# Kernel tuning notes

Measured on AMD Instinct MI355X. Metric: run time of the kernel, lower is better.

## Reference

```python
import jax, jax.numpy as jnp
import numpy as np

D = 256      # input channels
DK = 64      # key/query/value channels
BS, W, H = 8, 64, 64


def setup_inputs() -> dict:
    key = jax.random.key(0)
    k1, k2, k3, k4 = jax.random.split(key, 4)
    v = jax.random.normal(k1, (BS, D, W, H), dtype=jnp.float32)
    # conv1x1 weights collapse to plain matrices over the channel dim
    Wqkv = jax.random.normal(k2, (3 * DK, D), dtype=jnp.float32) * 0.02
    Wout = jax.random.normal(k3, (D, DK), dtype=jnp.float32) * 0.02
    gamma = jax.random.normal(k4, (1,), dtype=jnp.float32)  # original inits to 0; nonzero for a non-degenerate baseline
    return {"v": v, "Wqkv": Wqkv, "Wout": Wout, "gamma": gamma}


def reference(v, Wqkv, Wout, gamma):
    bs, c, w, h = v.shape
    n = w * h
    d_k = Wout.shape[1]
    x = v.reshape(bs, c, n)                      # (b, c, n)
    qkv = jnp.einsum('oc,bcn->bon', Wqkv, x)      # 1x1 conv == channel matmul
    q = qkv[:, :d_k]                              # (b, dk, n)
    k = qkv[:, d_k:2 * d_k]
    val = qkv[:, 2 * d_k:]
    s = jnp.einsum('bdi,bdj->bij', q, k)          # (b, n, n) = query^T key
    beta = jax.nn.softmax(s, axis=2)              # exp(s - logsumexp(s, axis=2))
    y = jnp.einsum('bdi,bij->bdj', val, beta)     # bmm(value, beta)
    o = jnp.einsum('od,bdn->bon', Wout, y) * gamma[0] + x
    return o.reshape(bs, c, w, h)
```

## Files before the change

kernel.cpp:

```cpp
#include <hip/hip_runtime.h>

typedef unsigned short ushort_t;
typedef __bf16 bf16x8 __attribute__((ext_vector_type(8)));
typedef short short4v __attribute__((ext_vector_type(4)));
typedef float f32x4 __attribute__((ext_vector_type(4)));
typedef unsigned int uint4v __attribute__((ext_vector_type(4)));
typedef unsigned int uint2v __attribute__((ext_vector_type(2)));

#define NTOK 4096
#define DMODEL 256
#define DK 64
#define BS 8
#define LN2INV 1.44269504088896f

__device__ __forceinline__ ushort_t f2bf(float f) {
  unsigned u = __builtin_bit_cast(unsigned, f);
  u += 0x7fffu + ((u >> 16) & 1u);
  return (ushort_t)(u >> 16);
}
__device__ __forceinline__ float bf2f(ushort_t s) {
  return __builtin_bit_cast(float, ((unsigned)s) << 16);
}
__device__ __forceinline__ bf16x8 lds_frag(const ushort_t* p) {
  return __builtin_bit_cast(bf16x8, *(const uint4v*)p);
}
__device__ __forceinline__ bf16x8 ldg8(const ushort_t* p) {
  return __builtin_bit_cast(bf16x8, *(const uint4v*)p);
}
__device__ __forceinline__ short4v lo8(uint4v v) {
  uint2v t; t.x = v.x; t.y = v.y;
  return __builtin_bit_cast(short4v, t);
}
__device__ __forceinline__ short4v hi8(uint4v v) {
  uint2v t; t.x = v.z; t.y = v.w;
  return __builtin_bit_cast(short4v, t);
}
__device__ __forceinline__ float fexp2(float x) {
#if __has_builtin(__builtin_amdgcn_exp2f)
  return __builtin_amdgcn_exp2f(x);
#else
  return exp2f(x);
#endif
}
__device__ __forceinline__ unsigned bfpack(float x, float y) {
  return __builtin_amdgcn_perm(__builtin_bit_cast(unsigned, y),
                               __builtin_bit_cast(unsigned, x), 0x07060302u);
}
__device__ __forceinline__ f32x4 mfma16(short4v a, short4v b, f32x4 c) {
#if defined(__HIP_DEVICE_COMPILE__)
#if __has_builtin(__builtin_amdgcn_mfma_f32_16x16x16bf16_1k)
  return __builtin_amdgcn_mfma_f32_16x16x16bf16_1k(a, b, c, 0, 0, 0);
#else
  typedef __bf16 bf16x4 __attribute__((ext_vector_type(4)));
  return __builtin_amdgcn_mfma_f32_16x16x16_bf16(__builtin_bit_cast(bf16x4, a),
                                                 __builtin_bit_cast(bf16x4, b), c, 0, 0, 0);
#endif
#else
  (void)a; (void)b;
  return c;
#endif
}

__global__ __launch_bounds__(256) void k_convert(const float* __restrict__ Wqkv,
                                                 const float* __restrict__ Wout,
                                                 ushort_t* __restrict__ Wb,
                                                 ushort_t* __restrict__ Woutb) {
  int i = blockIdx.x * 256 + threadIdx.x;
  if (i < 3 * DK * DMODEL) {
    float w = Wqkv[i];
    if (i < DK * DMODEL) w *= LN2INV;
    Wb[i] = f2bf(w);
  } else {
    int j = i - 3 * DK * DMODEL;
    Woutb[j] = f2bf(Wout[j]);
  }
}

__global__ __launch_bounds__(256) void k_transpose(const float* __restrict__ x,
                                                   ushort_t* __restrict__ xT) {
  const int b = blockIdx.z;
  const int c0 = blockIdx.y * 64;
  const int n0 = blockIdx.x * 64;
  const int tid = threadIdx.x;
  __shared__ __align__(16) ushort_t t[64 * 72];
  const float* xb = x + (size_t)b * DMODEL * NTOK;
  ushort_t* xTb = xT + (size_t)b * NTOK * DMODEL;
#pragma unroll
  for (int kr = 0; kr < 2; kr++) {
    int s = tid + 256 * kr;
    int c = s >> 3, ns = (s & 7) * 8;
    const float* src = xb + (size_t)(c0 + c) * NTOK + n0 + ns;
    f32x4 a = *(const f32x4*)src;
    f32x4 bq = *(const f32x4*)(src + 4);
    uint4v o;
    o.x = (unsigned)f2bf(a[0]) | ((unsigned)f2bf(a[1]) << 16);
    o.y = (unsigned)f2bf(a[2]) | ((unsigned)f2bf(a[3]) << 16);
    o.z = (unsigned)f2bf(bq[0]) | ((unsigned)f2bf(bq[1]) << 16);
    o.w = (unsigned)f2bf(bq[2]) | ((unsigned)f2bf(bq[3]) << 16);
    *(uint4v*)(t + c * 72 + ns) = o;
  }
  __syncthreads();
#pragma unroll
  for (int kr = 0; kr < 2; kr++) {
    int s = tid + 256 * kr;
    int n = s >> 3, cs = (s & 7) * 8;
    unsigned e0 = t[(cs + 0) * 72 + n], e1 = t[(cs + 1) * 72 + n];
    unsigned e2 = t[(cs + 2) * 72 + n], e3 = t[(cs + 3) * 72 + n];
    unsigned e4 = t[(cs + 4) * 72 + n], e5 = t[(cs + 5) * 72 + n];
    unsigned e6 = t[(cs + 6) * 72 + n], e7 = t[(cs + 7) * 72 + n];
    uint4v o;
    o.x = e0 | (e1 << 16); o.y = e2 | (e3 << 16);
    o.z = e4 | (e5 << 16); o.w = e6 | (e7 << 16);
    *(uint4v*)(xTb + (size_t)(n0 + n) * DMODEL + c0 + cs) = o;
  }
}

__global__ __launch_bounds__(256) void k_qkv(const ushort_t* __restrict__ xT,
                                             const ushort_t* __restrict__ W,
                                             ushort_t* __restrict__ QT,
                                             ushort_t* __restrict__ KT,
                                             ushort_t* __restrict__ Vf) {
  const int b = blockIdx.y;
  const int n0 = blockIdx.x * 64;
  const int tid = threadIdx.x;
  const int lane = tid & 63, wv = tid >> 6;
  const int quad = lane >> 4, l15 = lane & 15;
  __shared__ __align__(16) ushort_t lx[64 * 264];

  const ushort_t* xTb = xT + ((size_t)b * NTOK + n0) * DMODEL;
  {
    int n = tid >> 2, cseg = (tid & 3) * 64;
#pragma unroll
    for (int k = 0; k < 8; k++)
      *(uint4v*)(lx + n * 264 + cseg + k * 8) =
          *(const uint4v*)(xTb + (size_t)n * DMODEL + cseg + k * 8);
  }
  __syncthreads();

  f32x4 acc[3][4];
  const f32x4 zero4 = {0.f, 0.f, 0.f, 0.f};
#pragma unroll
  for (int i = 0; i < 3; i++)
#pragma unroll
    for (int j = 0; j < 4; j++) acc[i][j] = zero4;

#pragma unroll
  for (int c0 = 0; c0 < DMODEL; c0 += 32) {
    bf16x8 aw[3];
#pragma unroll
    for (int mt = 0; mt < 3; mt++)
      aw[mt] = ldg8(W + (wv * 48 + mt * 16 + l15) * DMODEL + c0 + quad * 8);
    bf16x8 bb[4];
#pragma unroll
    for (int nt = 0; nt < 4; nt++)
      bb[nt] = lds_frag(lx + (nt * 16 + l15) * 264 + c0 + quad * 8);
#pragma unroll
    for (int mt = 0; mt < 3; mt++)
#pragma unroll
      for (int nt = 0; nt < 4; nt++)
        acc[mt][nt] = __builtin_amdgcn_mfma_f32_16x16x32_bf16(aw[mt], bb[nt], acc[mt][nt], 0, 0, 0);
  }

#pragma unroll
  for (int mt = 0; mt < 3; mt++) {
    int o = wv * 48 + mt * 16 + quad * 4;
#pragma unroll
    for (int nt = 0; nt < 4; nt++) {
      int n = n0 + nt * 16 + l15;
      f32x4 v4 = acc[mt][nt];
      if (o < 128) {
        ushort_t* dst = (o < 64) ? (QT + ((size_t)b * NTOK + n) * DK + o)
                                 : (KT + ((size_t)b * NTOK + n) * DK + (o - 64));
        uint2v ww;
        ww.x = (unsigned)f2bf(v4[0]) | ((unsigned)f2bf(v4[1]) << 16);
        ww.y = (unsigned)f2bf(v4[2]) | ((unsigned)f2bf(v4[3]) << 16);
        *(uint2v*)dst = ww;
      } else {
        int dbase = o - 128;
        size_t tbase = ((((size_t)b * 64 + (n0 >> 6)) * 4 + nt) * 2 + (dbase >> 5)) * 512;
        ushort_t* vp = Vf + tbase + ((l15 >> 2) << 7) + ((dbase & 15) << 3) +
                       (((dbase >> 4) & 1) << 2) + (l15 & 3);
#pragma unroll
        for (int r = 0; r < 4; r++) vp[r << 3] = f2bf(v4[r]);
      }
    }
  }
}

__global__ __launch_bounds__(256, 4) void k_rsum(const ushort_t* __restrict__ QT,
                                                 const ushort_t* __restrict__ KT,
                                                 float* __restrict__ Rp) {
  const int id = blockIdx.x;
  const int b = id & 7;
  const int rest = id >> 3;
  const int i0 = (rest & 63) * 64;
  const int jh = rest >> 6;
  const int tid = threadIdx.x;
  const int lane = tid & 63, wv = tid >> 6;
  const int quad = lane >> 4, l15 = lane & 15;
  const ushort_t* QTb = QT + ((size_t)b * NTOK + i0) * DK;
  const ushort_t* KTb = KT + ((size_t)b * NTOK + jh * 2048 + wv * 512) * DK;

  bf16x8 aq0[4], aq1[4];
#pragma unroll
  for (int isub = 0; isub < 4; isub++) {
    const ushort_t* qp = QTb + (size_t)(isub * 16 + l15) * DK + quad * 8;
    aq0[isub] = ldg8(qp);
    aq1[isub] = ldg8(qp + 32);
  }

  f32x4 racc[4];
  const f32x4 zero4 = {0.f, 0.f, 0.f, 0.f};
#pragma unroll
  for (int isub = 0; isub < 4; isub++) racc[isub] = zero4;

#pragma unroll 1
  for (int ph = 0; ph < 8; ph++) {
    const ushort_t* kb_base = KTb + (size_t)ph * 64 * DK;
    bf16x8 kb0[4], kb1[4];
#pragma unroll
    for (int nt = 0; nt < 4; nt++) {
      const ushort_t* kp = kb_base + (size_t)(nt * 16 + l15) * DK + quad * 8;
      kb0[nt] = ldg8(kp);
      kb1[nt] = ldg8(kp + 32);
    }
#pragma unroll
    for (int isub = 0; isub < 4; isub++)
#pragma unroll
      for (int nt = 0; nt < 4; nt++) {
        f32x4 s4 = __builtin_amdgcn_mfma_f32_16x16x32_bf16(aq0[isub], kb0[nt], zero4, 0, 0, 0);
        s4 = __builtin_amdgcn_mfma_f32_16x16x32_bf16(aq1[isub], kb1[nt], s4, 0, 0, 0);
        racc[isub][0] += fexp2(s4[0]);
        racc[isub][1] += fexp2(s4[1]);
        racc[isub][2] += fexp2(s4[2]);
        racc[isub][3] += fexp2(s4[3]);
      }
  }

#pragma unroll
  for (int isub = 0; isub < 4; isub++)
#pragma unroll
    for (int r = 0; r < 4; r++) {
      float v = racc[isub][r];
      v += __shfl_xor(v, 1);
      v += __shfl_xor(v, 2);
      v += __shfl_xor(v, 4);
      v += __shfl_xor(v, 8);
      racc[isub][r] = v;
    }
  if (l15 == 0) {
    float* dst = Rp + ((size_t)(jh * 4 + wv) * BS + b) * NTOK + i0;
#pragma unroll
    for (int isub = 0; isub < 4; isub++)
      *(f32x4*)(dst + isub * 16 + quad * 4) = racc[isub];
  }
}

__global__ __launch_bounds__(256) void k_rmerge(const float* __restrict__ Rp,
                                                float* __restrict__ Rr) {
  int g = blockIdx.x * 256 + threadIdx.x;
  float s = 0.f;
#pragma unroll
  for (int p = 0; p < 8; p++) s += Rp[(size_t)p * BS * NTOK + g];
  Rr[g] = -__log2f(s);
}

__global__ __launch_bounds__(256, 3) void k_pv(const ushort_t* __restrict__ QT,
                                               const ushort_t* __restrict__ KT,
                                               const ushort_t* __restrict__ Vf,
                                               const float* __restrict__ Rr,
                                               ushort_t* __restrict__ Yp) {
  const int id = blockIdx.x;
  const int b = id & 7;
  const int rest = id >> 3;
  const int j0 = (rest & 63) * 64;
  const int ih = rest >> 6;
  const int tid = threadIdx.x;
  const int lane = tid & 63, wv = tid >> 6;
  const int quad = lane >> 4, l15 = lane & 15;

  __shared__ __align__(16) ushort_t pool[13312];
  float* rbuf = (float*)pool;
  ushort_t* pbuf = pool + 8704;

  const ushort_t* KTb = KT + ((size_t)b * NTOK + j0) * DK;
  const ushort_t* QTb = QT + ((size_t)b * NTOK + ih * 2048) * DK;
  const ushort_t* Vfb = Vf + ((size_t)b * 64 + ih * 32) * 4096;
  const float* Rrb = Rr + (size_t)b * NTOK + ih * 2048;

  bf16x8 kb0[4], kb1[4];
#pragma unroll
  for (int nt = 0; nt < 4; nt++) {
    const ushort_t* kp = KTb + (size_t)(nt * 16 + l15) * DK + quad * 8;
    kb0[nt] = ldg8(kp);
    kb1[nt] = ldg8(kp + 32);
  }

  f32x4 yt[4][4];
  const f32x4 zero4 = {0.f, 0.f, 0.f, 0.f};
#pragma unroll
  for (int i = 0; i < 4; i++)
#pragma unroll
    for (int j = 0; j < 4; j++) yt[i][j] = zero4;

  const int qrow = (wv * 16 + l15) * DK + quad * 8;
  const int vfo = wv * 1024 + lane * 8;

#pragma unroll 2
  for (int it = 0; it < 32; it++) {
    const ushort_t* qp = QTb + (size_t)it * 64 * DK + qrow;
    bf16x8 a0 = ldg8(qp);
    bf16x8 a1 = ldg8(qp + 32);
    const ushort_t* vp = Vfb + (size_t)it * 4096 + vfo;
    uint4v vv0 = *(const uint4v*)vp;
    uint4v vv1 = *(const uint4v*)(vp + 512);
    f32x4 lrv = *(const f32x4*)(Rrb + it * 64 + wv * 16 + quad * 4);
    short4v vf0 = lo8(vv0), vf1 = hi8(vv0), vf2 = lo8(vv1), vf3 = hi8(vv1);
#pragma unroll
    for (int nt = 0; nt < 4; nt++) {
      f32x4 s4 = __builtin_amdgcn_mfma_f32_16x16x32_bf16(a0, kb0[nt], lrv, 0, 0, 0);
      s4 = __builtin_amdgcn_mfma_f32_16x16x32_bf16(a1, kb1[nt], s4, 0, 0, 0);
      uint2v wp;
      wp.x = bfpack(fexp2(s4[0]), fexp2(s4[1]));
      wp.y = bfpack(fexp2(s4[2]), fexp2(s4[3]));
      short4v wf = __builtin_bit_cast(short4v, wp);
      yt[nt][0] = mfma16(wf, vf0, yt[nt][0]);
      yt[nt][1] = mfma16(wf, vf1, yt[nt][1]);
      yt[nt][2] = mfma16(wf, vf2, yt[nt][2]);
      yt[nt][3] = mfma16(wf, vf3, yt[nt][3]);
    }
  }

  if (wv == 0) {
#pragma unroll
    for (int nt = 0; nt < 4; nt++)
#pragma unroll
      for (int dsub = 0; dsub < 4; dsub++)
        *(f32x4*)(rbuf + (dsub * 16 + l15) * 68 + nt * 16 + quad * 4) = yt[nt][dsub];
  }
  __syncthreads();
  if (wv == 1) {
#pragma unroll
    for (int nt = 0; nt < 4; nt++)
#pragma unroll
      for (int dsub = 0; dsub < 4; dsub++) {
        float* p = rbuf + (dsub * 16 + l15) * 68 + nt * 16 + quad * 4;
        *(f32x4*)p = *(const f32x4*)p + yt[nt][dsub];
      }
  }
  __syncthreads();
  if (wv == 2) {
#pragma unroll
    for (int nt = 0; nt < 4; nt++)
#pragma unroll
      for (int dsub = 0; dsub < 4; dsub++) {
        float* p = rbuf + (dsub * 16 + l15) * 68 + nt * 16 + quad * 4;
        *(f32x4*)p = *(const f32x4*)p + yt[nt][dsub];
      }
  }
  __syncthreads();
  if (wv == 3) {
#pragma unroll
    for (int nt = 0; nt < 4; nt++)
#pragma unroll
      for (int dsub = 0; dsub < 4; dsub++) {
        const float* p = rbuf + (dsub * 16 + l15) * 68 + nt * 16 + quad * 4;
        f32x4 v4 = *(const f32x4*)p + yt[nt][dsub];
#pragma unroll
        for (int r = 0; r < 4; r++)
          pbuf[(nt * 16 + quad * 4 + r) * 72 + dsub * 16 + l15] = f2bf(v4[r]);
      }
  }
  __syncthreads();

  ushort_t* Ypb = Yp + ((size_t)(ih * 8 + b) * NTOK + j0) * DK;
#pragma unroll
  for (int kr = 0; kr < 2; kr++) {
    int s = tid + 256 * kr;
    int row = s >> 3, cc = (s & 7) * 8;
    *(uint4v*)(Ypb + (size_t)row * DK + cc) = *(const uint4v*)(pbuf + row * 72 + cc);
  }
}

__global__ __launch_bounds__(256) void k_out(const ushort_t* __restrict__ Yp,
                                             const ushort_t* __restrict__ Wout,
                                             const float* __restrict__ gammap,
                                             const float* __restrict__ x,
                                             float* __restrict__ outp) {
  const int id = blockIdx.x;
  const int b = id & 7;
  const int n0 = (id >> 3) * 64;
  const int tid = threadIdx.x;
  const int lane = tid & 63, wv = tid >> 6;
  const int quad = lane >> 4, l15 = lane & 15;
  __shared__ __align__(16) ushort_t pbuf[64 * 72];

  const ushort_t* Y0 = Yp + ((size_t)b * NTOK + n0) * DK;
  const ushort_t* Y1 = Yp + ((size_t)(8 + b) * NTOK + n0) * DK;
#pragma unroll
  for (int kr = 0; kr < 2; kr++) {
    int s = tid + 256 * kr;
    int row = s >> 3, c8 = (s & 7) * 8;
    uint4v ua = *(const uint4v*)(Y0 + (size_t)row * DK + c8);
    uint4v ub = *(const uint4v*)(Y1 + (size_t)row * DK + c8);
    uint4v oc;
    unsigned* pa = (unsigned*)&ua;
    unsigned* pb = (unsigned*)&ub;
    unsigned* po = (unsigned*)&oc;
#pragma unroll
    for (int w = 0; w < 4; w++) {
      float lo = bf2f((ushort_t)(pa[w] & 0xffff)) + bf2f((ushort_t)(pb[w] & 0xffff));
      float hi = bf2f((ushort_t)(pa[w] >> 16)) + bf2f((ushort_t)(pb[w] >> 16));
      po[w] = bfpack(lo, hi);
    }
    *(uint4v*)(pbuf + row * 72 + c8) = oc;
  }
  __syncthreads();

  const f32x4 zero4 = {0.f, 0.f, 0.f, 0.f};
  bf16x8 yb0[4], yb1[4];
#pragma unroll
  for (int nt = 0; nt < 4; nt++) {
    yb0[nt] = lds_frag(pbuf + (nt * 16 + l15) * 72 + quad * 8);
    yb1[nt] = lds_frag(pbuf + (nt * 16 + l15) * 72 + 32 + quad * 8);
  }
  f32x4 oacc[4][4];
#pragma unroll
  for (int m = 0; m < 4; m++)
#pragma unroll
    for (int nt = 0; nt < 4; nt++) oacc[m][nt] = zero4;
#pragma unroll
  for (int m = 0; m < 4; m++) {
    int c = (wv * 4 + m) * 16 + l15;
    bf16x8 aw0 = __builtin_bit_cast(bf16x8, *(const uint4v*)(Wout + c * DK + quad * 8));
    bf16x8 aw1 = __builtin_bit_cast(bf16x8, *(const uint4v*)(Wout + c * DK + 32 + quad * 8));
#pragma unroll
    for (int nt = 0; nt < 4; nt++) {
      oacc[m][nt] = __builtin_amdgcn_mfma_f32_16x16x32_bf16(aw0, yb0[nt], oacc[m][nt], 0, 0, 0);
      oacc[m][nt] = __builtin_amdgcn_mfma_f32_16x16x32_bf16(aw1, yb1[nt], oacc[m][nt], 0, 0, 0);
    }
  }
  float g = gammap[0];
  const float* xb = x + (size_t)b * DMODEL * NTOK;
  float* ob = outp + (size_t)b * DMODEL * NTOK;
#pragma unroll
  for (int m = 0; m < 4; m++) {
    int cbase = (wv * 4 + m) * 16 + quad * 4;
#pragma unroll
    for (int nt = 0; nt < 4; nt++) {
      int n = n0 + nt * 16 + l15;
#pragma unroll
      for (int r = 0; r < 4; r++) {
        size_t idx = (size_t)(cbase + r) * NTOK + n;
        ob[idx] = oacc[m][nt][r] * g + xb[idx];
      }
    }
  }
}

extern "C" void kernel_launch(void* const* d_in, const int* in_sizes, int n_in,
                              void* d_out, int out_size, void* d_ws, size_t ws_size,
                              hipStream_t stream) {
  const float* v = (const float*)d_in[0];
  const float* Wqkv = (const float*)d_in[1];
  const float* Wout = (const float*)d_in[2];
  const float* gamma = (const float*)d_in[3];
  float* outp = (float*)d_out;

  ushort_t* xT = (ushort_t*)d_ws;
  ushort_t* QT = xT + (size_t)BS * NTOK * DMODEL;
  ushort_t* KT = QT + (size_t)BS * NTOK * DK;
  ushort_t* Vf = KT + (size_t)BS * NTOK * DK;
  ushort_t* Wb = Vf + (size_t)BS * DK * NTOK;
  ushort_t* Woutb = Wb + 3 * DK * DMODEL;
  float* RpOld = (float*)(Woutb + DMODEL * DK);
  float* Rr = RpOld + 2 * (size_t)BS * NTOK;
  ushort_t* Yp = (ushort_t*)(Rr + (size_t)BS * NTOK);
  float* Rp = (float*)xT;

  k_convert<<<dim3(256), 256, 0, stream>>>(Wqkv, Wout, Wb, Woutb);
  k_transpose<<<dim3(64, 4, BS), 256, 0, stream>>>(v, xT);
  k_qkv<<<dim3(64, BS), 256, 0, stream>>>(xT, Wb, QT, KT, Vf);
  k_rsum<<<dim3(1024), 256, 0, stream>>>(QT, KT, Rp);
  k_rmerge<<<dim3(128), 256, 0, stream>>>(Rp, Rr);
  k_pv<<<dim3(1024), 256, 0, stream>>>(QT, KT, Vf, Rr, Yp);
  k_out<<<dim3(512), 256, 0, stream>>>(Yp, Woutb, gamma, v, outp);
}
```

Baseline: 222.5 us.

## Fuse transpose into QKV projection, merge row-sum reduction, retune PV occupancy

The separate fp32-to-bf16 transpose kernel is folded into the QKV projection kernel, which now transposes each 64-channel chunk through shared memory straight into its operand tile. This removes the round trip of the transposed input through global memory. The row-sum kernel now uses 512-thread blocks that each cover all 4096 keys and reduce the eight wave partials in shared memory before writing -log2 of the sum, which eliminates the separate merge kernel and its partial buffer. The PV kernel's launch bound goes from 3 to 4 blocks per SM and its unroll from 2 to 1, trading instruction-level overlap for occupancy.

```diff
diff --git a/kernel.cpp b/kernel.cpp
--- a/kernel.cpp
+++ b/kernel.cpp
@@ -76,46 +76,7 @@
   }
 }
 
-__global__ __launch_bounds__(256) void k_transpose(const float* __restrict__ x,
-                                                   ushort_t* __restrict__ xT) {
-  const int b = blockIdx.z;
-  const int c0 = blockIdx.y * 64;
-  const int n0 = blockIdx.x * 64;
-  const int tid = threadIdx.x;
-  __shared__ __align__(16) ushort_t t[64 * 72];
-  const float* xb = x + (size_t)b * DMODEL * NTOK;
-  ushort_t* xTb = xT + (size_t)b * NTOK * DMODEL;
-#pragma unroll
-  for (int kr = 0; kr < 2; kr++) {
-    int s = tid + 256 * kr;
-    int c = s >> 3, ns = (s & 7) * 8;
-    const float* src = xb + (size_t)(c0 + c) * NTOK + n0 + ns;
-    f32x4 a = *(const f32x4*)src;
-    f32x4 bq = *(const f32x4*)(src + 4);
-    uint4v o;
-    o.x = (unsigned)f2bf(a[0]) | ((unsigned)f2bf(a[1]) << 16);
-    o.y = (unsigned)f2bf(a[2]) | ((unsigned)f2bf(a[3]) << 16);
-    o.z = (unsigned)f2bf(bq[0]) | ((unsigned)f2bf(bq[1]) << 16);
-    o.w = (unsigned)f2bf(bq[2]) | ((unsigned)f2bf(bq[3]) << 16);
-    *(uint4v*)(t + c * 72 + ns) = o;
-  }
-  __syncthreads();
-#pragma unroll
-  for (int kr = 0; kr < 2; kr++) {
-    int s = tid + 256 * kr;
-    int n = s >> 3, cs = (s & 7) * 8;
-    unsigned e0 = t[(cs + 0) * 72 + n], e1 = t[(cs + 1) * 72 + n];
-    unsigned e2 = t[(cs + 2) * 72 + n], e3 = t[(cs + 3) * 72 + n];
-    unsigned e4 = t[(cs + 4) * 72 + n], e5 = t[(cs + 5) * 72 + n];
-    unsigned e6 = t[(cs + 6) * 72 + n], e7 = t[(cs + 7) * 72 + n];
-    uint4v o;
-    o.x = e0 | (e1 << 16); o.y = e2 | (e3 << 16);
-    o.z = e4 | (e5 << 16); o.w = e6 | (e7 << 16);
-    *(uint4v*)(xTb + (size_t)(n0 + n) * DMODEL + c0 + cs) = o;
-  }
-}
-
-__global__ __launch_bounds__(256) void k_qkv(const ushort_t* __restrict__ xT,
+__global__ __launch_bounds__(256) void k_qkv(const float* __restrict__ x,
                                              const ushort_t* __restrict__ W,
                                              ushort_t* __restrict__ QT,
                                              ushort_t* __restrict__ KT,
@@ -126,16 +87,43 @@
   const int lane = tid & 63, wv = tid >> 6;
   const int quad = lane >> 4, l15 = lane & 15;
   __shared__ __align__(16) ushort_t lx[64 * 264];
-
-  const ushort_t* xTb = xT + ((size_t)b * NTOK + n0) * DMODEL;
-  {
-    int n = tid >> 2, cseg = (tid & 3) * 64;
-#pragma unroll
-    for (int k = 0; k < 8; k++)
-      *(uint4v*)(lx + n * 264 + cseg + k * 8) =
-          *(const uint4v*)(xTb + (size_t)n * DMODEL + cseg + k * 8);
-  }
-  __syncthreads();
+  __shared__ __align__(16) ushort_t t[64 * 72];
+
+  const float* xb = x + (size_t)b * DMODEL * NTOK;
+
+#pragma unroll 1
+  for (int cc = 0; cc < 4; cc++) {
+    const int c0chunk = cc * 64;
+#pragma unroll
+    for (int kr = 0; kr < 2; kr++) {
+      int s = tid + 256 * kr;
+      int c = s >> 3, ns = (s & 7) * 8;
+      const float* src = xb + (size_t)(c0chunk + c) * NTOK + n0 + ns;
+      f32x4 a = *(const f32x4*)src;
+      f32x4 bq = *(const f32x4*)(src + 4);
+      uint4v o;
+      o.x = (unsigned)f2bf(a[0]) | ((unsigned)f2bf(a[1]) << 16);
+      o.y = (unsigned)f2bf(a[2]) | ((unsigned)f2bf(a[3]) << 16);
+      o.z = (unsigned)f2bf(bq[0]) | ((unsigned)f2bf(bq[1]) << 16);
+      o.w = (unsigned)f2bf(bq[2]) | ((unsigned)f2bf(bq[3]) << 16);
+      *(uint4v*)(t + c * 72 + ns) = o;
+    }
+    __syncthreads();
+#pragma unroll
+    for (int kr = 0; kr < 2; kr++) {
+      int s = tid + 256 * kr;
+      int n = s >> 3, cs = (s & 7) * 8;
+      unsigned e0 = t[(cs + 0) * 72 + n], e1 = t[(cs + 1) * 72 + n];
+      unsigned e2 = t[(cs + 2) * 72 + n], e3 = t[(cs + 3) * 72 + n];
+      unsigned e4 = t[(cs + 4) * 72 + n], e5 = t[(cs + 5) * 72 + n];
+      unsigned e6 = t[(cs + 6) * 72 + n], e7 = t[(cs + 7) * 72 + n];
+      uint4v o;
+      o.x = e0 | (e1 << 16); o.y = e2 | (e3 << 16);
+      o.z = e4 | (e5 << 16); o.w = e6 | (e7 << 16);
+      *(uint4v*)(lx + n * 264 + c0chunk + cs) = o;
+    }
+    __syncthreads();
+  }
 
   f32x4 acc[3][4];
   const f32x4 zero4 = {0.f, 0.f, 0.f, 0.f};
@@ -187,19 +175,18 @@
   }
 }
 
-__global__ __launch_bounds__(256, 4) void k_rsum(const ushort_t* __restrict__ QT,
+__global__ __launch_bounds__(512, 4) void k_rsum(const ushort_t* __restrict__ QT,
                                                  const ushort_t* __restrict__ KT,
-                                                 float* __restrict__ Rp) {
+                                                 float* __restrict__ Rr) {
   const int id = blockIdx.x;
   const int b = id & 7;
-  const int rest = id >> 3;
-  const int i0 = (rest & 63) * 64;
-  const int jh = rest >> 6;
+  const int i0 = (id >> 3) * 64;
   const int tid = threadIdx.x;
   const int lane = tid & 63, wv = tid >> 6;
   const int quad = lane >> 4, l15 = lane & 15;
+  __shared__ __align__(16) float partial[8 * 64];
   const ushort_t* QTb = QT + ((size_t)b * NTOK + i0) * DK;
-  const ushort_t* KTb = KT + ((size_t)b * NTOK + jh * 2048 + wv * 512) * DK;
+  const ushort_t* KTb = KT + ((size_t)b * NTOK + wv * 512) * DK;
 
   bf16x8 aq0[4], aq1[4];
 #pragma unroll
@@ -249,23 +236,20 @@
       racc[isub][r] = v;
     }
   if (l15 == 0) {
-    float* dst = Rp + ((size_t)(jh * 4 + wv) * BS + b) * NTOK + i0;
 #pragma unroll
     for (int isub = 0; isub < 4; isub++)
-      *(f32x4*)(dst + isub * 16 + quad * 4) = racc[isub];
-  }
-}
-
-__global__ __launch_bounds__(256) void k_rmerge(const float* __restrict__ Rp,
-                                                float* __restrict__ Rr) {
-  int g = blockIdx.x * 256 + threadIdx.x;
-  float s = 0.f;
-#pragma unroll
-  for (int p = 0; p < 8; p++) s += Rp[(size_t)p * BS * NTOK + g];
-  Rr[g] = -__log2f(s);
-}
-
-__global__ __launch_bounds__(256, 3) void k_pv(const ushort_t* __restrict__ QT,
+      *(f32x4*)(partial + wv * 64 + isub * 16 + quad * 4) = racc[isub];
+  }
+  __syncthreads();
+  if (tid < 64) {
+    float s = 0.f;
+#pragma unroll
+    for (int w = 0; w < 8; w++) s += partial[w * 64 + tid];
+    Rr[(size_t)b * NTOK + i0 + tid] = -__log2f(s);
+  }
+}
+
+__global__ __launch_bounds__(256, 4) void k_pv(const ushort_t* __restrict__ QT,
                                                const ushort_t* __restrict__ KT,
                                                const ushort_t* __restrict__ Vf,
                                                const float* __restrict__ Rr,
@@ -306,7 +290,7 @@
   const int qrow = (wv * 16 + l15) * DK + quad * 8;
   const int vfo = wv * 1024 + lane * 8;
 
-#pragma unroll 2
+#pragma unroll 1
   for (int it = 0; it < 32; it++) {
     const ushort_t* qp = QTb + (size_t)it * 64 * DK + qrow;
     bf16x8 a0 = ldg8(qp);
@@ -467,22 +451,17 @@
   const float* gamma = (const float*)d_in[3];
   float* outp = (float*)d_out;
 
-  ushort_t* xT = (ushort_t*)d_ws;
-  ushort_t* QT = xT + (size_t)BS * NTOK * DMODEL;
+  ushort_t* QT = (ushort_t*)d_ws;
   ushort_t* KT = QT + (size_t)BS * NTOK * DK;
   ushort_t* Vf = KT + (size_t)BS * NTOK * DK;
   ushort_t* Wb = Vf + (size_t)BS * DK * NTOK;
   ushort_t* Woutb = Wb + 3 * DK * DMODEL;
-  float* RpOld = (float*)(Woutb + DMODEL * DK);
-  float* Rr = RpOld + 2 * (size_t)BS * NTOK;
+  float* Rr = (float*)(Woutb + DMODEL * DK);
   ushort_t* Yp = (ushort_t*)(Rr + (size_t)BS * NTOK);
-  float* Rp = (float*)xT;
 
   k_convert<<<dim3(256), 256, 0, stream>>>(Wqkv, Wout, Wb, Woutb);
-  k_transpose<<<dim3(64, 4, BS), 256, 0, stream>>>(v, xT);
-  k_qkv<<<dim3(64, BS), 256, 0, stream>>>(xT, Wb, QT, KT, Vf);
-  k_rsum<<<dim3(1024), 256, 0, stream>>>(QT, KT, Rp);
-  k_rmerge<<<dim3(128), 256, 0, stream>>>(Rp, Rr);
+  k_qkv<<<dim3(64, BS), 256, 0, stream>>>(v, Wb, QT, KT, Vf);
+  k_rsum<<<dim3(512), 512, 0, stream>>>(QT, KT, Rr);
   k_pv<<<dim3(1024), 256, 0, stream>>>(QT, KT, Vf, Rr, Yp);
   k_out<<<dim3(512), 256, 0, stream>>>(Yp, Woutb, gamma, v, outp);
 }
```

After: 203.9 us. 1.09x faster.
